# Kernel tuning notes

Hardware: AMD Instinct MI355X
Metric: run time of the kernel (lower is better)

The kernel has to match this reference:

```python
import jax, jax.numpy as jnp
import numpy as np

B, N, DIM = 16, 1024, 512
H, KD, D = 16, 32, 128          # num_heads, key_dim, d = attn_ratio*key_dim
DH = H * D                      # 2048
HQKV = DH + 2 * H * KD          # 3072
RES = 32
SCALE = KD ** -0.5
EPS = 1e-5


def _make_bias_idxs():
    ii = np.arange(N)
    px, py = ii // RES, ii % RES
    dx = np.abs(px[:, None] - px[None, :])
    dy = np.abs(py[:, None] - py[None, :])
    return (dx * RES + dy).astype(np.int32)  # (N, N), values in [0, RES*RES)


def setup_inputs() -> dict:
    key = jax.random.key(0)
    ks = jax.random.split(key, 6)
    return {
        "x": jax.random.normal(ks[0], (B, N, DIM), jnp.float32),
        "gamma": jnp.ones((DIM,), jnp.float32),
        "beta": jnp.zeros((DIM,), jnp.float32),
        "qkv_w": jax.random.normal(ks[1], (HQKV, DIM), jnp.float32) * 0.02,
        "qkv_b": jax.random.normal(ks[2], (HQKV,), jnp.float32) * 0.02,
        "proj_w": jax.random.normal(ks[3], (DIM, DH), jnp.float32) * 0.02,
        "proj_b": jax.random.normal(ks[4], (DIM,), jnp.float32) * 0.02,
        "attention_biases": jax.random.normal(ks[5], (H, RES * RES), jnp.float32) * 0.02,
        "bias_idxs": jnp.asarray(_make_bias_idxs()),
    }


def reference(x, gamma, beta, qkv_w, qkv_b, proj_w, proj_b, attention_biases, bias_idxs):
    # LayerNorm
    mu = jnp.mean(x, axis=-1, keepdims=True)
    var = jnp.mean(jnp.square(x - mu), axis=-1, keepdims=True)
    xn = (x - mu) * jax.lax.rsqrt(var + EPS) * gamma + beta
    # QKV projection -> (B, H, N, kd+kd+d)
    qkv = (xn @ qkv_w.T + qkv_b).reshape(B, N, H, 2 * KD + D).transpose(0, 2, 1, 3)
    q, k, v = qkv[..., :KD], qkv[..., KD:2 * KD], qkv[..., 2 * KD:]
    # Relative-position bias gather: (H, N, N)
    bias = attention_biases[:, bias_idxs]
    attn = jnp.einsum("bhnk,bhmk->bhnm", q, k) * SCALE + bias
    attn = jax.nn.softmax(attn, axis=-1)
    out = jnp.einsum("bhnm,bhmd->bhnd", attn, v)  # (B, H, N, D)
    out = out.transpose(0, 2, 1, 3).reshape(B, N, DH)
    return out @ proj_w.T + proj_b
```

## Files before the change

kernel.cpp:

```cpp
#include <hip/hip_runtime.h>

#define DIM_   512
#define NSEQ   1024
#define BB     16
#define HH     16
#define KD_    32
#define DD_    128
#define LDQKV  3072
#define DH_    2048
#define SCALE_ 0.17677669529663687f

typedef __bf16 bf16x8 __attribute__((ext_vector_type(8)));
typedef float  f32x4  __attribute__((ext_vector_type(4)));
typedef unsigned int u32x4v __attribute__((ext_vector_type(4)));

typedef __attribute__((address_space(1))) const unsigned int guint;
typedef __attribute__((address_space(3))) unsigned int luint;
#define GLL16(gp, lp) __builtin_amdgcn_global_load_lds((guint*)(gp), (luint*)(lp), 16, 0, 0)

static __device__ __forceinline__ unsigned short f2bf(float f) {
  unsigned int u = __builtin_bit_cast(unsigned int, f);
  u += 0x7fffu + ((u >> 16) & 1u);
  return (unsigned short)(u >> 16);
}

__global__ __launch_bounds__(256) void cvt_kernel(const float* __restrict__ in,
                                                  unsigned short* __restrict__ out,
                                                  int n) {
  int i = blockIdx.x * 256 + threadIdx.x;
  if (i < n) out[i] = f2bf(in[i]);
}

__global__ __launch_bounds__(256) void ln_kernel(const float* __restrict__ x,
                                                 const float* __restrict__ gamma,
                                                 const float* __restrict__ beta,
                                                 unsigned short* __restrict__ xn) {
  int row = blockIdx.x, t = threadIdx.x;
  const float* xr = x + (size_t)row * DIM_;
  float2 v = *(const float2*)(xr + t * 2);
  float s = v.x + v.y, sq = v.x * v.x + v.y * v.y;
#pragma unroll
  for (int off = 32; off; off >>= 1) {
    s  += __shfl_xor(s, off, 64);
    sq += __shfl_xor(sq, off, 64);
  }
  __shared__ float red[8];
  int wid = t >> 6, lane = t & 63;
  if (lane == 0) { red[wid * 2] = s; red[wid * 2 + 1] = sq; }
  __syncthreads();
  float S  = red[0] + red[2] + red[4] + red[6];
  float SQ = red[1] + red[3] + red[5] + red[7];
  float mu   = S * (1.f / DIM_);
  float var  = SQ * (1.f / DIM_) - mu * mu;
  float rstd = rsqrtf(var + 1e-5f);
  int c = t * 2;
  xn[(size_t)row * DIM_ + c]     = f2bf((v.x - mu) * rstd * gamma[c]     + beta[c]);
  xn[(size_t)row * DIM_ + c + 1] = f2bf((v.y - mu) * rstd * gamma[c + 1] + beta[c + 1]);
}

template <typename OUT, bool VREMAP>
__global__ __launch_bounds__(256) void gemm_gll(const unsigned short* __restrict__ A, int lda,
                                                const unsigned short* __restrict__ W, int ldb,
                                                const float* __restrict__ bias,
                                                OUT* __restrict__ C, int ldc,
                                                int K) {
  __shared__ unsigned short a_sm[128][64];
  __shared__ unsigned short b_sm[128][64];
  int tid = threadIdx.x;
  int lane = tid & 63, w = tid >> 6;
  int quad = lane >> 4, l15 = lane & 15;
  int wr = w >> 1, wc = w & 1;
  long tm = (long)blockIdx.y * 128, tn = (long)blockIdx.x * 128;
  int srow = w * 8 + (lane >> 3), scol = (lane & 7) * 8;

  f32x4 acc[4][4] = {};

  for (int k0 = 0; k0 < K; k0 += 64) {
    __syncthreads();
#pragma unroll
    for (int it = 0; it < 4; it++) {
      if constexpr (VREMAP) {
        int kk = k0 + scol;
        GLL16(A + (size_t)(tm + it * 32 + srow) * LDQKV + (kk >> 7) * 192 + 64 + (kk & 127),
              &a_sm[it * 32 + w * 8][0]);
      } else {
        GLL16(A + (tm + it * 32 + srow) * lda + k0 + scol, &a_sm[it * 32 + w * 8][0]);
      }
      GLL16(W + (tn + it * 32 + srow) * ldb + k0 + scol, &b_sm[it * 32 + w * 8][0]);
    }
    __syncthreads();
#pragma unroll
    for (int kk = 0; kk < 64; kk += 32) {
      bf16x8 af[4], bfr[4];
#pragma unroll
      for (int i = 0; i < 4; i++)
        af[i] = *(const bf16x8*)&a_sm[wr * 64 + i * 16 + l15][kk + quad * 8];
#pragma unroll
      for (int j = 0; j < 4; j++)
        bfr[j] = *(const bf16x8*)&b_sm[wc * 64 + j * 16 + l15][kk + quad * 8];
#pragma unroll
      for (int i = 0; i < 4; i++)
#pragma unroll
        for (int j = 0; j < 4; j++)
          acc[i][j] = __builtin_amdgcn_mfma_f32_16x16x32_bf16(af[i], bfr[j], acc[i][j], 0, 0, 0);
    }
  }
#pragma unroll
  for (int j = 0; j < 4; j++) {
    long col = tn + wc * 64 + j * 16 + l15;
    float bv = bias[col];
#pragma unroll
    for (int i = 0; i < 4; i++) {
      long row0 = tm + wr * 64 + i * 16 + quad * 4;
#pragma unroll
      for (int r = 0; r < 4; r++) {
        float val = acc[i][j][r] + bv;
        if constexpr (__is_same(OUT, float))
          C[(row0 + r) * ldc + col] = val;
        else
          C[(row0 + r) * ldc + col] = f2bf(val);
      }
    }
  }
}

__global__ __launch_bounds__(256) void transpose_v(const unsigned short* __restrict__ qkv,
                                                   unsigned short* __restrict__ vT) {
  __shared__ unsigned short lt[128][64];
  int tid = threadIdx.x;
  int nt = blockIdx.x, bh = blockIdx.y;
  int b = bh >> 4, h = bh & 15;
  const unsigned short* src = qkv + ((size_t)b * NSEQ + nt * 64) * LDQKV + h * 192 + 64;
#pragma unroll
  for (int i = 0; i < 4; i++) {
    int u = tid + 256 * i;
    int nl = u >> 4, d8 = u & 15;
    uint4 r = *(const uint4*)(src + (size_t)nl * LDQKV + d8 * 8);
    const unsigned short* pr = (const unsigned short*)&r;
#pragma unroll
    for (int e = 0; e < 8; e++)
      lt[d8 * 8 + e][nl ^ ((d8 & 7) * 8)] = pr[e];
  }
  __syncthreads();
  unsigned short* dst = vT + (size_t)bh * 131072 + nt * 64;
#pragma unroll
  for (int i = 0; i < 4; i++) {
    int u = tid + 256 * i;
    int d = u >> 3, p = u & 7;
    int ct = p ^ ((d >> 3) & 7);
    *(uint4*)(dst + (size_t)d * 1024 + ct * 8) = *(const uint4*)&lt[d][p * 8];
  }
}

__global__ __launch_bounds__(256) void attn_kernel(const unsigned short* __restrict__ qkv,
                                                   const unsigned short* __restrict__ vT,
                                                   const float* __restrict__ ab,
                                                   unsigned short* attn_out) {
  __shared__ float lut[1024];
  __shared__ unsigned short v_sm[128][64];
  __shared__ unsigned short k_sm[64][32];

  int tid = threadIdx.x;
  int lane = tid & 63, w = tid >> 6;
  int quad = lane >> 4, l15 = lane & 15;

  int id = blockIdx.x;
  int bh = ((id >> 7) << 3) | (id & 7);
  int qb = (id >> 3) & 15;
  int b = bh >> 4, h = bh & 15;
  const unsigned short* base = qkv + (size_t)b * NSEQ * LDQKV + h * 192;
  const unsigned short* vTh = vT + (size_t)bh * 131072;

  for (int t = tid; t < 1024; t += 256) lut[t] = ab[h * 1024 + t];

  int qg = qb * 64 + w * 16 + l15;
  bf16x8 qf = *(const bf16x8*)(base + (size_t)qg * LDQKV + quad * 8);

  int rx = qg >> 5, ry = qg & 31;
  int dy_pre[8];
#pragma unroll
  for (int i = 0; i < 8; i++) {
    int cy = ((i >> 2) << 4) | (quad * 4 + (i & 3));
    int d = ry - cy; dy_pre[i] = d < 0 ? -d : d;
  }

  int ixA = ((quad & 1) * 32 + l15) * 4;
  int ixB = ixA + 64;
  bool hiq = quad >= 2;

  f32x4 accO[8] = {};
  float l_r = 0.f;

  int vrow   = lane >> 3;
  int vchunk = (lane & 7) ^ (lane >> 3);
  int krow   = w * 16 + (lane >> 2);
  int kcol   = (lane & 3) * 8;

  for (int kt = 0; kt < 16; kt++) {
    __syncthreads();
#pragma unroll
    for (int i = 0; i < 4; i++) {
      int r0 = (w * 4 + i) * 8;
      GLL16(vTh + (size_t)(r0 + vrow) * 1024 + kt * 64 + vchunk * 8, &v_sm[r0][0]);
    }
    GLL16(base + (size_t)(kt * 64 + krow) * LDQKV + 32 + kcol, &k_sm[w * 16][0]);
    asm volatile("s_waitcnt vmcnt(0)");
    __syncthreads();

    f32x4 st[4];
#pragma unroll
    for (int nb = 0; nb < 4; nb++) {
      bf16x8 kf = *(const bf16x8*)&k_sm[nb * 16 + l15][quad * 8];
      f32x4 z = {};
      st[nb] = __builtin_amdgcn_mfma_f32_16x16x32_bf16(kf, qf, z, 0, 0, 0);
    }

    int d0 = rx - 2 * kt;     int dxa = d0 < 0 ? -d0 : d0;
    int d1 = d0 - 1;          int dxb = d1 < 0 ? -d1 : d1;
    int lb0 = dxa << 5, lb1 = dxb << 5;

    unsigned pk[8];
#pragma unroll
    for (int nb = 0; nb < 4; nb++) {
      int lb = (nb & 2) ? lb1 : lb0;
#pragma unroll
      for (int t = 0; t < 2; t++) {
        float p0 = __expf(fmaf(st[nb][2 * t],     SCALE_, lut[lb + dy_pre[(nb & 1) * 4 + 2 * t]]));
        float p1 = __expf(fmaf(st[nb][2 * t + 1], SCALE_, lut[lb + dy_pre[(nb & 1) * 4 + 2 * t + 1]]));
        l_r += p0 + p1;
        unsigned short u0 = __builtin_bit_cast(unsigned short, (__bf16)p0);
        unsigned short u1 = __builtin_bit_cast(unsigned short, (__bf16)p1);
        pk[nb * 2 + t] = (unsigned)u0 | ((unsigned)u1 << 16);
      }
    }

#pragma unroll
    for (int kc = 0; kc < 2; kc++) {
      int s0 = (int)pk[4 * kc + 0], s1 = (int)pk[4 * kc + 1];
      int s2 = (int)pk[4 * kc + 2], s3 = (int)pk[4 * kc + 3];
      unsigned a0 = (unsigned)__builtin_amdgcn_ds_bpermute(ixA, s0);
      unsigned a1 = (unsigned)__builtin_amdgcn_ds_bpermute(ixA, s1);
      unsigned a2 = (unsigned)__builtin_amdgcn_ds_bpermute(ixA, s2);
      unsigned a3 = (unsigned)__builtin_amdgcn_ds_bpermute(ixA, s3);
      unsigned b0 = (unsigned)__builtin_amdgcn_ds_bpermute(ixB, s0);
      unsigned b1 = (unsigned)__builtin_amdgcn_ds_bpermute(ixB, s1);
      unsigned b2 = (unsigned)__builtin_amdgcn_ds_bpermute(ixB, s2);
      unsigned b3 = (unsigned)__builtin_amdgcn_ds_bpermute(ixB, s3);
      u32x4v paw;
      paw.x = hiq ? a2 : a0;
      paw.y = hiq ? a3 : a1;
      paw.z = hiq ? b2 : b0;
      paw.w = hiq ? b3 : b1;
      bf16x8 paf = __builtin_bit_cast(bf16x8, paw);

#pragma unroll
      for (int db = 0; db < 8; db++) {
        bf16x8 vf = *(const bf16x8*)&v_sm[db * 16 + l15][((kc * 4 + quad) ^ (l15 & 7)) * 8];
        accO[db] = __builtin_amdgcn_mfma_f32_16x16x32_bf16(paf, vf, accO[db], 0, 0, 0);
      }
    }
  }

  l_r += __shfl_xor(l_r, 16, 64);
  l_r += __shfl_xor(l_r, 32, 64);

#pragma unroll
  for (int r = 0; r < 4; r++) {
    float lr = __shfl(l_r, quad * 4 + r, 16);
    float inv = 1.f / lr;
    int row = qb * 64 + w * 16 + quad * 4 + r;
    size_t obase = ((size_t)b * NSEQ + row) * LDQKV + h * 192 + 64;
#pragma unroll
    for (int db = 0; db < 8; db++)
      attn_out[obase + db * 16 + l15] = f2bf(accO[db][r] * inv);
  }
}

extern "C" void kernel_launch(void* const* d_in, const int* in_sizes, int n_in,
                              void* d_out, int out_size, void* d_ws, size_t ws_size,
                              hipStream_t stream) {
  const float* x      = (const float*)d_in[0];
  const float* gamma  = (const float*)d_in[1];
  const float* beta   = (const float*)d_in[2];
  const float* qkv_w  = (const float*)d_in[3];
  const float* qkv_b  = (const float*)d_in[4];
  const float* proj_w = (const float*)d_in[5];
  const float* proj_b = (const float*)d_in[6];
  const float* ab     = (const float*)d_in[7];

  char* ws = (char*)d_ws;
  unsigned short* xn    = (unsigned short*)(ws);
  unsigned short* wqkv  = (unsigned short*)(ws + (size_t)16 * 1048576);
  unsigned short* wproj = (unsigned short*)(ws + (size_t)19 * 1048576);
  unsigned short* qkv   = (unsigned short*)(ws + (size_t)21 * 1048576);
  unsigned short* vT    = (unsigned short*)(ws + (size_t)117 * 1048576);
  float* out = (float*)d_out;

  cvt_kernel<<<dim3(6144), dim3(256), 0, stream>>>(qkv_w, wqkv, 3072 * 512);
  cvt_kernel<<<dim3(4096), dim3(256), 0, stream>>>(proj_w, wproj, 512 * 2048);
  ln_kernel<<<dim3(16384), dim3(256), 0, stream>>>(x, gamma, beta, xn);
  gemm_gll<unsigned short, false><<<dim3(24, 128), dim3(256), 0, stream>>>(xn, 512, wqkv, 512, qkv_b, qkv, 3072, 512);
  transpose_v<<<dim3(16, 256), dim3(256), 0, stream>>>(qkv, vT);
  attn_kernel<<<dim3(4096), dim3(256), 0, stream>>>(qkv, vT, ab, qkv);
  gemm_gll<float, true><<<dim3(4, 128), dim3(256), 0, stream>>>(qkv, 3072, wproj, 2048, proj_b, out, 512, 2048);
}
```

Before: 449.5 us.

## Process two query tiles per attention block and compute row sums via MFMA

Each attention workgroup now handles 128 query rows, as two 64-row groups, instead of 64. The K and V tiles staged in LDS are reused across both groups, which halves global-to-LDS traffic and the grid size. The per-row softmax denominator is now accumulated with an extra MFMA against a ones vector, replacing the scalar adds and cross-lane shuffles. In exchange, register pressure roughly doubles for the accumulators, which may lower occupancy, and the row sum now uses the bf16-rounded probabilities.

Result: slower. 524.1 us (+16.6%).

```diff
diff --git a/kernel.cpp b/kernel.cpp
--- a/kernel.cpp
+++ b/kernel.cpp
@@ -165,18 +165,20 @@
   int quad = lane >> 4, l15 = lane & 15;
 
   int id = blockIdx.x;
-  int bh = ((id >> 7) << 3) | (id & 7);
-  int qb = (id >> 3) & 15;
+  int bh = ((id >> 6) << 3) | (id & 7);
+  int qb = (id >> 3) & 7;
   int b = bh >> 4, h = bh & 15;
   const unsigned short* base = qkv + (size_t)b * NSEQ * LDQKV + h * 192;
   const unsigned short* vTh = vT + (size_t)bh * 131072;
 
   for (int t = tid; t < 1024; t += 256) lut[t] = ab[h * 1024 + t];
 
-  int qg = qb * 64 + w * 16 + l15;
-  bf16x8 qf = *(const bf16x8*)(base + (size_t)qg * LDQKV + quad * 8);
-
-  int rx = qg >> 5, ry = qg & 31;
+  int qg0 = qb * 128 + w * 16 + l15;
+  bf16x8 qf[2];
+  qf[0] = *(const bf16x8*)(base + (size_t)qg0 * LDQKV + quad * 8);
+  qf[1] = *(const bf16x8*)(base + (size_t)(qg0 + 64) * LDQKV + quad * 8);
+
+  int rx = qg0 >> 5, ry = qg0 & 31;
   int dy_pre[8];
 #pragma unroll
   for (int i = 0; i < 8; i++) {
@@ -188,8 +190,11 @@
   int ixB = ixA + 64;
   bool hiq = quad >= 2;
 
-  f32x4 accO[8] = {};
-  float l_r = 0.f;
+  u32x4v ow; ow.x = ow.y = ow.z = ow.w = 0x3F803F80u;
+  const bf16x8 onesf = __builtin_bit_cast(bf16x8, ow);
+
+  f32x4 accO[2][8] = {};
+  f32x4 accL[2] = {};
 
   int vrow   = lane >> 3;
   int vchunk = (lane & 7) ^ (lane >> 3);
@@ -207,72 +212,82 @@
     asm volatile("s_waitcnt vmcnt(0)");
     __syncthreads();
 
-    f32x4 st[4];
-#pragma unroll
-    for (int nb = 0; nb < 4; nb++) {
-      bf16x8 kf = *(const bf16x8*)&k_sm[nb * 16 + l15][quad * 8];
-      f32x4 z = {};
-      st[nb] = __builtin_amdgcn_mfma_f32_16x16x32_bf16(kf, qf, z, 0, 0, 0);
-    }
-
-    int d0 = rx - 2 * kt;     int dxa = d0 < 0 ? -d0 : d0;
-    int d1 = d0 - 1;          int dxb = d1 < 0 ? -d1 : d1;
-    int lb0 = dxa << 5, lb1 = dxb << 5;
-
-    unsigned pk[8];
-#pragma unroll
-    for (int nb = 0; nb < 4; nb++) {
-      int lb = (nb & 2) ? lb1 : lb0;
-#pragma unroll
-      for (int t = 0; t < 2; t++) {
-        float p0 = __expf(fmaf(st[nb][2 * t],     SCALE_, lut[lb + dy_pre[(nb & 1) * 4 + 2 * t]]));
-        float p1 = __expf(fmaf(st[nb][2 * t + 1], SCALE_, lut[lb + dy_pre[(nb & 1) * 4 + 2 * t + 1]]));
-        l_r += p0 + p1;
-        unsigned short u0 = __builtin_bit_cast(unsigned short, (__bf16)p0);
-        unsigned short u1 = __builtin_bit_cast(unsigned short, (__bf16)p1);
-        pk[nb * 2 + t] = (unsigned)u0 | ((unsigned)u1 << 16);
+    int d0 = rx - 2 * kt;
+    int e0 = d0,     lbA0 = (e0 < 0 ? -e0 : e0) << 5;
+    int e1 = d0 - 1; int lbB0 = (e1 < 0 ? -e1 : e1) << 5;
+    int e2 = d0 + 2; int lbA1 = (e2 < 0 ? -e2 : e2) << 5;
+    int e3 = d0 + 1; int lbB1 = (e3 < 0 ? -e3 : e3) << 5;
+
+    unsigned pk[2][8];
+#pragma unroll
+    for (int g = 0; g < 2; g++) {
+      f32x4 st[4];
+#pragma unroll
+      for (int nb = 0; nb < 4; nb++) {
+        bf16x8 kf = *(const bf16x8*)&k_sm[nb * 16 + l15][quad * 8];
+        f32x4 z = {};
+        st[nb] = __builtin_amdgcn_mfma_f32_16x16x32_bf16(kf, qf[g], z, 0, 0, 0);
+      }
+      int lbA = g ? lbA1 : lbA0;
+      int lbB = g ? lbB1 : lbB0;
+#pragma unroll
+      for (int nb = 0; nb < 4; nb++) {
+        int lb = (nb & 2) ? lbB : lbA;
+#pragma unroll
+        for (int t = 0; t < 2; t++) {
+          float p0 = __expf(fmaf(st[nb][2 * t],     SCALE_, lut[lb + dy_pre[(nb & 1) * 4 + 2 * t]]));
+          float p1 = __expf(fmaf(st[nb][2 * t + 1], SCALE_, lut[lb + dy_pre[(nb & 1) * 4 + 2 * t + 1]]));
+          unsigned short u0 = __builtin_bit_cast(unsigned short, (__bf16)p0);
+          unsigned short u1 = __builtin_bit_cast(unsigned short, (__bf16)p1);
+          pk[g][nb * 2 + t] = (unsigned)u0 | ((unsigned)u1 << 16);
+        }
       }
     }
 
 #pragma unroll
     for (int kc = 0; kc < 2; kc++) {
-      int s0 = (int)pk[4 * kc + 0], s1 = (int)pk[4 * kc + 1];
-      int s2 = (int)pk[4 * kc + 2], s3 = (int)pk[4 * kc + 3];
-      unsigned a0 = (unsigned)__builtin_amdgcn_ds_bpermute(ixA, s0);
-      unsigned a1 = (unsigned)__builtin_amdgcn_ds_bpermute(ixA, s1);
-      unsigned a2 = (unsigned)__builtin_amdgcn_ds_bpermute(ixA, s2);
-      unsigned a3 = (unsigned)__builtin_amdgcn_ds_bpermute(ixA, s3);
-      unsigned b0 = (unsigned)__builtin_amdgcn_ds_bpermute(ixB, s0);
-      unsigned b1 = (unsigned)__builtin_amdgcn_ds_bpermute(ixB, s1);
-      unsigned b2 = (unsigned)__builtin_amdgcn_ds_bpermute(ixB, s2);
-      unsigned b3 = (unsigned)__builtin_amdgcn_ds_bpermute(ixB, s3);
-      u32x4v paw;
-      paw.x = hiq ? a2 : a0;
-      paw.y = hiq ? a3 : a1;
-      paw.z = hiq ? b2 : b0;
-      paw.w = hiq ? b3 : b1;
-      bf16x8 paf = __builtin_bit_cast(bf16x8, paw);
-
+      bf16x8 paf[2];
+#pragma unroll
+      for (int g = 0; g < 2; g++) {
+        int s0 = (int)pk[g][4 * kc + 0], s1 = (int)pk[g][4 * kc + 1];
+        int s2 = (int)pk[g][4 * kc + 2], s3 = (int)pk[g][4 * kc + 3];
+        unsigned a0 = (unsigned)__builtin_amdgcn_ds_bpermute(ixA, s0);
+        unsigned a1 = (unsigned)__builtin_amdgcn_ds_bpermute(ixA, s1);
+        unsigned a2 = (unsigned)__builtin_amdgcn_ds_bpermute(ixA, s2);
+        unsigned a3 = (unsigned)__builtin_amdgcn_ds_bpermute(ixA, s3);
+        unsigned b0 = (unsigned)__builtin_amdgcn_ds_bpermute(ixB, s0);
+        unsigned b1 = (unsigned)__builtin_amdgcn_ds_bpermute(ixB, s1);
+        unsigned b2 = (unsigned)__builtin_amdgcn_ds_bpermute(ixB, s2);
+        unsigned b3 = (unsigned)__builtin_amdgcn_ds_bpermute(ixB, s3);
+        u32x4v paw;
+        paw.x = hiq ? a2 : a0;
+        paw.y = hiq ? a3 : a1;
+        paw.z = hiq ? b2 : b0;
+        paw.w = hiq ? b3 : b1;
+        paf[g] = __builtin_bit_cast(bf16x8, paw);
+      }
 #pragma unroll
       for (int db = 0; db < 8; db++) {
         bf16x8 vf = *(const bf16x8*)&v_sm[db * 16 + l15][((kc * 4 + quad) ^ (l15 & 7)) * 8];
-        accO[db] = __builtin_amdgcn_mfma_f32_16x16x32_bf16(paf, vf, accO[db], 0, 0, 0);
-      }
-    }
-  }
-
-  l_r += __shfl_xor(l_r, 16, 64);
-  l_r += __shfl_xor(l_r, 32, 64);
-
-#pragma unroll
-  for (int r = 0; r < 4; r++) {
-    float lr = __shfl(l_r, quad * 4 + r, 16);
-    float inv = 1.f / lr;
-    int row = qb * 64 + w * 16 + quad * 4 + r;
-    size_t obase = ((size_t)b * NSEQ + row) * LDQKV + h * 192 + 64;
-#pragma unroll
-    for (int db = 0; db < 8; db++)
-      attn_out[obase + db * 16 + l15] = f2bf(accO[db][r] * inv);
+        accO[0][db] = __builtin_amdgcn_mfma_f32_16x16x32_bf16(paf[0], vf, accO[0][db], 0, 0, 0);
+        accO[1][db] = __builtin_amdgcn_mfma_f32_16x16x32_bf16(paf[1], vf, accO[1][db], 0, 0, 0);
+      }
+      accL[0] = __builtin_amdgcn_mfma_f32_16x16x32_bf16(paf[0], onesf, accL[0], 0, 0, 0);
+      accL[1] = __builtin_amdgcn_mfma_f32_16x16x32_bf16(paf[1], onesf, accL[1], 0, 0, 0);
+    }
+  }
+
+#pragma unroll
+  for (int g = 0; g < 2; g++) {
+#pragma unroll
+    for (int r = 0; r < 4; r++) {
+      float inv = 1.f / accL[g][r];
+      int row = qb * 128 + g * 64 + w * 16 + quad * 4 + r;
+      size_t obase = ((size_t)b * NSEQ + row) * LDQKV + h * 192 + 64;
+#pragma unroll
+      for (int db = 0; db < 8; db++)
+        attn_out[obase + db * 16 + l15] = f2bf(accO[g][db][r] * inv);
+    }
   }
 }
 
@@ -301,6 +316,6 @@
   ln_kernel<<<dim3(16384), dim3(256), 0, stream>>>(x, gamma, beta, xn);
   gemm_gll<unsigned short, false><<<dim3(24, 128), dim3(256), 0, stream>>>(xn, 512, wqkv, 512, qkv_b, qkv, 3072, 512);
   transpose_v<<<dim3(16, 256), dim3(256), 0, stream>>>(qkv, vT);
-  attn_kernel<<<dim3(4096), dim3(256), 0, stream>>>(qkv, vT, ab, qkv);
+  attn_kernel<<<dim3(2048), dim3(256), 0, stream>>>(qkv, vT, ab, qkv);
   gemm_gll<float, true><<<dim3(4, 128), dim3(256), 0, stream>>>(qkv, 3072, wproj, 2048, proj_b, out, 512, 2048);
 }
```
